# Performance work log

Hardware: AMD Instinct MI355X
Metric: run time of the kernel (lower is better)

## Reference

```python
import jax, jax.numpy as jnp
import numpy as np

B_SZ, L, H, P, V, OUT_LEN = 32, 4096, 512, 384, 32, 16
DT_MIN, DT_MAX = 0.001, 0.1


def setup_inputs() -> dict:
    key = jax.random.key(0)
    ks = jax.random.split(key, 12)
    tokens = jax.random.randint(ks[0], (B_SZ, L), 0, V, dtype=jnp.int32)
    embed = jax.random.normal(ks[1], (V, H), dtype=jnp.float32) * 0.02
    # S5 diagonal state: Lambda = Lambda_re + i*Lambda_im (stable: Re < 0)
    Lambda_re = -0.5 * jax.random.uniform(ks[2], (P,), dtype=jnp.float32) - 1e-3
    Lambda_im = jnp.pi * jnp.arange(P, dtype=jnp.float32)
    B_re = jax.random.normal(ks[3], (P, H), dtype=jnp.float32) / np.sqrt(H)
    B_im = jax.random.normal(ks[4], (P, H), dtype=jnp.float32) / np.sqrt(H)
    C_re = jax.random.normal(ks[5], (H, P), dtype=jnp.float32) / np.sqrt(P)
    C_im = jax.random.normal(ks[6], (H, P), dtype=jnp.float32) / np.sqrt(P)
    D = jax.random.normal(ks[7], (H,), dtype=jnp.float32)
    log_step = jax.random.uniform(
        ks[8], (P,), dtype=jnp.float32,
        minval=np.log(DT_MIN), maxval=np.log(DT_MAX))
    W1 = jax.random.normal(ks[9], (H, H), dtype=jnp.float32) / np.sqrt(H)
    b1 = jnp.zeros((H,), dtype=jnp.float32)
    W2 = jax.random.normal(ks[10], (H, V), dtype=jnp.float32) / np.sqrt(H)
    b2 = jnp.zeros((V,), dtype=jnp.float32)
    return dict(tokens=tokens, embed=embed, Lambda_re=Lambda_re,
                Lambda_im=Lambda_im, B_re=B_re, B_im=B_im, C_re=C_re,
                C_im=C_im, D=D, log_step=log_step, W1=W1, b1=b1, W2=W2, b2=b2)


def _s5_scan(Lbar, Bu_bar):
    # Lbar: (P,) complex; Bu_bar: (B,L,P) complex
    A = jnp.broadcast_to(Lbar, Bu_bar.shape)

    def comb(e1, e2):
        A1, b1 = e1
        A2, b2 = e2
        return A2 * A1, A2 * b1 + b2

    _, xs = jax.lax.associative_scan(comb, (A, Bu_bar), axis=1)
    return xs  # (B,L,P) hidden states


def reference(tokens, embed, Lambda_re, Lambda_im, B_re, B_im,
              C_re, C_im, D, log_step, W1, b1, W2, b2):
    u = embed[tokens]                              # (B,L,H) real
    Lam = Lambda_re + 1j * Lambda_im               # (P,)
    step = jnp.exp(log_step)                       # (P,)
    Lbar = jnp.exp(Lam * step)                     # ZOH: exp(Lambda*dt)
    Bc = B_re + 1j * B_im                          # (P,H)
    Cc = C_re + 1j * C_im                          # (H,P)
    Bu = jnp.einsum('blh,ph->blp', u, Bc)          # (B,L,P) complex
    Bu_bar = ((Lbar - 1.0) / Lam) * Bu             # ZOH input discretization
    xs = _s5_scan(Lbar, Bu_bar)                    # (B,L,P)
    # conj_sym=True -> 2 * Re(C x) + D u
    y = 2.0 * jnp.einsum('blp,hp->blh', xs, Cc).real + u * D
    y = y[:, -OUT_LEN:, :]                         # (B,16,H)
    h = jax.nn.relu(y @ W1 + b1)
    return h @ W2 + b2                             # (B,16,V)
```

## Files before the change

kernel.cpp:

```cpp
#include <hip/hip_runtime.h>

#define B_SZ 32
#define L 4096
#define H 512
#define P 384
#define V 32
#define OUT_LEN 16
#define NSC 12
#define SCLEN 340
#define NSTEP 85
#define T0 4080

#define OFF_DBL   0
#define OFF_LBF4  4608
#define OFF_WPOW  5376
#define OFF_M     23808
#define OFF_CT    48384
#define OFF_XACC  441600
#define OFF_YT    466176
#define OFF_HP    728320

__global__ __launch_bounds__(256) void k_prep(
    const float* __restrict__ embed,
    const float* __restrict__ Lre, const float* __restrict__ Lim,
    const float* __restrict__ Bre, const float* __restrict__ Bim,
    const float* __restrict__ Cre, const float* __restrict__ Cim,
    const float* __restrict__ log_step, float* __restrict__ ws)
{
    __shared__ float sre[32][33], sim[32][33];
    int bx = blockIdx.x, tid = threadIdx.x;
    if (bx < 96) ws[OFF_XACC + bx * 256 + tid] = 0.f;
    if (bx < 2) {
        int p = bx * 256 + tid;
        if (p < P) {
            double dstep = exp((double)log_step[p]);
            double are = (double)Lre[p] * dstep, aim = (double)Lim[p] * dstep;
            double mag = exp(are);
            double lbr = mag * cos(aim), lbi = mag * sin(aim);
            double lre = (double)Lre[p], lim = (double)Lim[p];
            double nr = lbr - 1.0, ni = lbi;
            double den = lre * lre + lim * lim;
            double cr = (nr * lre + ni * lim) / den, ci = (ni * lre - nr * lim) / den;
            double* d = (double*)ws + p * 6;
            d[0] = lbr; d[1] = lbi; d[2] = 0.0; d[3] = 0.0; d[4] = cr; d[5] = ci;
            double m4 = exp(4.0 * are), a4 = 4.0 * aim;
            ws[OFF_LBF4 + 2 * p]     = (float)(m4 * cos(a4));
            ws[OFF_LBF4 + 2 * p + 1] = (float)(m4 * sin(a4));
            double wmag = exp((double)SCLEN * are);
            double wang = (double)SCLEN * aim;
            double wr = wmag * cos(wang), wi = wmag * sin(wang);
            double* wpow = (double*)(ws + OFF_WPOW);
            double awr = 1.0, awi = 0.0;
            for (int c = NSC - 1; c >= 0; --c) {
                wpow[(c * P + p) * 2]     = awr;
                wpow[(c * P + p) * 2 + 1] = awi;
                double t = awr * wr - awi * wi;
                awi = awr * wi + awi * wr;
                awr = t;
            }
        }
    } else if (bx < 194) {
        int bxx = bx - 2;
        int tp = bxx >> 4, th = bxx & 15;
        int col = tid & 31, r0 = tid >> 5;
        #pragma unroll
        for (int it = 0; it < 4; ++it) {
            int row = r0 + 8 * it;
            int h = th * 32 + row, p = tp * 32 + col;
            sre[col][row] = Cre[h * P + p];
            sim[col][row] = Cim[h * P + p];
        }
        __syncthreads();
        #pragma unroll
        for (int it = 0; it < 4; ++it) {
            int pl = r0 + 8 * it;
            int p = tp * 32 + pl, h = th * 32 + col;
            ws[OFF_CT + (2 * p) * H + h]     = sre[pl][col];
            ws[OFF_CT + (2 * p + 1) * H + h] = sim[pl][col];
        }
    }
    {
        int w = bx * 4 + (tid >> 6);
        if (w < 1536) {
            int v0 = (w & 3) * 8, p = w >> 2;
            int lane = tid & 63;
            const float4* brp = (const float4*)(Bre + p * H);
            const float4* bip = (const float4*)(Bim + p * H);
            float4 br0 = brp[lane], br1 = brp[lane + 64];
            float4 bi0 = bip[lane], bi1 = bip[lane + 64];
            #pragma unroll
            for (int vv = 0; vv < 8; ++vv) {
                const float4* evp = (const float4*)(embed + (v0 + vv) * H);
                float4 e0 = evp[lane], e1 = evp[lane + 64];
                float dr = br0.x * e0.x;
                dr = fmaf(br0.y, e0.y, dr); dr = fmaf(br0.z, e0.z, dr);
                dr = fmaf(br0.w, e0.w, dr); dr = fmaf(br1.x, e1.x, dr);
                dr = fmaf(br1.y, e1.y, dr); dr = fmaf(br1.z, e1.z, dr);
                dr = fmaf(br1.w, e1.w, dr);
                float di = bi0.x * e0.x;
                di = fmaf(bi0.y, e0.y, di); di = fmaf(bi0.z, e0.z, di);
                di = fmaf(bi0.w, e0.w, di); di = fmaf(bi1.x, e1.x, di);
                di = fmaf(bi1.y, e1.y, di); di = fmaf(bi1.z, e1.z, di);
                di = fmaf(bi1.w, e1.w, di);
                #pragma unroll
                for (int off = 32; off; off >>= 1) {
                    dr += __shfl_down(dr, off);
                    di += __shfl_down(di, off);
                }
                if (lane == 0) {
                    ws[OFF_M + ((v0 + vv) * P + p) * 2]     = dr;
                    ws[OFF_M + ((v0 + vv) * P + p) * 2 + 1] = di;
                }
            }
        }
    }
}

__global__ __launch_bounds__(256) void k_scan(
    const int* __restrict__ tokens, float* __restrict__ ws)
{
    __shared__ float2 sM[V * 192];
    int x = blockIdx.x, b = blockIdx.y, tid = threadIdx.x;
    int ph = x & 1;
    int sc = x >> 1;
    const float2* Mg = (const float2*)(ws + OFF_M);
    for (int f = tid; f < V * 192; f += 256) {
        int v = f / 192, i = f - v * 192;
        sM[f] = Mg[v * P + ph * 192 + i];
    }
    __syncthreads();
    if (tid < 192) {
        int p = ph * 192 + tid;
        float Lr = ws[OFF_LBF4 + 2 * p], Li = ws[OFF_LBF4 + 2 * p + 1];
        const int4* tkb = (const int4*)(tokens + b * L + sc * SCLEN);
        float ar0 = 0, ai0 = 0, ar1 = 0, ai1 = 0;
        float ar2 = 0, ai2 = 0, ar3 = 0, ai3 = 0;
        int4 tq = tkb[0];
        #pragma unroll 5
        for (int i = 0; i < NSTEP; ++i) {
            int4 cur = tq;
            if (i + 1 < NSTEP) tq = tkb[i + 1];
            float2 m0 = sM[cur.x * 192 + tid];
            float2 m1 = sM[cur.y * 192 + tid];
            float2 m2 = sM[cur.z * 192 + tid];
            float2 m3 = sM[cur.w * 192 + tid];
            float n;
            n = fmaf(Lr, ar0, fmaf(-Li, ai0, m0.x));
            ai0 = fmaf(Lr, ai0, fmaf(Li, ar0, m0.y)); ar0 = n;
            n = fmaf(Lr, ar1, fmaf(-Li, ai1, m1.x));
            ai1 = fmaf(Lr, ai1, fmaf(Li, ar1, m1.y)); ar1 = n;
            n = fmaf(Lr, ar2, fmaf(-Li, ai2, m2.x));
            ai2 = fmaf(Lr, ai2, fmaf(Li, ar2, m2.y)); ar2 = n;
            n = fmaf(Lr, ar3, fmaf(-Li, ai3, m3.x));
            ai3 = fmaf(Lr, ai3, fmaf(Li, ar3, m3.y)); ar3 = n;
        }
        const double* d = (const double*)ws + p * 6;
        double l1r = d[0], l1i = d[1];
        double l2r = l1r * l1r - l1i * l1i, l2i = 2.0 * l1r * l1i;
        double l3r = l2r * l1r - l2i * l1i, l3i = l2r * l1i + l2i * l1r;
        double zr = l3r * ar0 - l3i * ai0 + l2r * ar1 - l2i * ai1
                  + l1r * ar2 - l1i * ai2 + (double)ar3;
        double zi = l3r * ai0 + l3i * ar0 + l2r * ai1 + l2i * ar1
                  + l1r * ai2 + l1i * ar2 + (double)ai3;
        const double* wpow = (const double*)(ws + OFF_WPOW);
        double wr = wpow[(sc * P + p) * 2], wi = wpow[(sc * P + p) * 2 + 1];
        float sr = (float)(wr * zr - wi * zi);
        float si = (float)(wr * zi + wi * zr);
        atomicAdd(ws + OFF_XACC + (b * P + p) * 2, sr);
        atomicAdd(ws + OFF_XACC + (b * P + p) * 2 + 1, si);
    }
}

__global__ __launch_bounds__(256) void k_y(
    const int* __restrict__ tokens, const float* __restrict__ embed,
    const float* __restrict__ D, float* __restrict__ ws)
{
    __shared__ __align__(16) float sxs[P * 20];
    __shared__ float sred[4 * 64 * 9];
    int bx = blockIdx.x, tid = threadIdx.x;
    int b = bx >> 4, x = bx & 15;
    int lh = x & 1, hq = x >> 1;
    #pragma unroll
    for (int pass = 0; pass < 2; ++pass) {
        int p = tid + pass * 256;
        if (p < P) {
            const double* d = (const double*)ws + p * 6;
            double lbr = d[0], lbi = d[1], cr = d[4], ci = d[5];
            const float2 za = *(const float2*)(ws + OFF_XACC + (b * P + p) * 2);
            double zr = (double)za.x, zi = (double)za.y;
            const float* M0 = ws + OFF_M;
            const int* tk = tokens + b * L + T0;
            #pragma unroll
            for (int j = 0; j < OUT_LEN; ++j) {
                int t = tk[j];
                double mr = (double)M0[(t * P + p) * 2];
                double mi = (double)M0[(t * P + p) * 2 + 1];
                double tr = lbr * zr - lbi * zi + mr;
                double ti = lbr * zi + lbi * zr + mi;
                zr = tr; zi = ti;
                if ((j >> 3) == lh) {
                    int jl = j & 7;
                    sxs[p * 20 + 2 * jl]     = (float)(cr * zr - ci * zi);
                    sxs[p * 20 + 2 * jl + 1] = (float)(cr * zi + ci * zr);
                }
            }
        }
    }
    __syncthreads();
    int hl = tid & 63, pg = tid >> 6;
    int h = hq * 64 + hl;
    const float* ct = ws + OFF_CT;
    float acc[8];
    #pragma unroll
    for (int i = 0; i < 8; ++i) acc[i] = 0.f;
    int p0 = pg * 96;
    float pr_[4], pi_[4];
    #pragma unroll
    for (int u = 0; u < 4; ++u) {
        pr_[u] = ct[(2 * (p0 + u)) * H + h];
        pi_[u] = ct[(2 * (p0 + u) + 1) * H + h];
    }
    for (int qs = 0; qs < 96; qs += 4) {
        float cr_[4], ci_[4];
        #pragma unroll
        for (int u = 0; u < 4; ++u) { cr_[u] = pr_[u]; ci_[u] = pi_[u]; }
        if (qs + 4 < 96) {
            #pragma unroll
            for (int u = 0; u < 4; ++u) {
                pr_[u] = ct[(2 * (p0 + qs + 4 + u)) * H + h];
                pi_[u] = ct[(2 * (p0 + qs + 4 + u) + 1) * H + h];
            }
        }
        #pragma unroll
        for (int u = 0; u < 4; ++u) {
            const float4* xv = (const float4*)(sxs + (p0 + qs + u) * 20);
            float4 x0 = xv[0], x1 = xv[1], x2 = xv[2], x3 = xv[3];
            float cre = cr_[u], cim = ci_[u];
            acc[0] = fmaf(cre, x0.x, fmaf(-cim, x0.y, acc[0]));
            acc[1] = fmaf(cre, x0.z, fmaf(-cim, x0.w, acc[1]));
            acc[2] = fmaf(cre, x1.x, fmaf(-cim, x1.y, acc[2]));
            acc[3] = fmaf(cre, x1.z, fmaf(-cim, x1.w, acc[3]));
            acc[4] = fmaf(cre, x2.x, fmaf(-cim, x2.y, acc[4]));
            acc[5] = fmaf(cre, x2.z, fmaf(-cim, x2.w, acc[5]));
            acc[6] = fmaf(cre, x3.x, fmaf(-cim, x3.y, acc[6]));
            acc[7] = fmaf(cre, x3.z, fmaf(-cim, x3.w, acc[7]));
        }
    }
    #pragma unroll
    for (int i = 0; i < 8; ++i)
        sred[(pg * 64 + hl) * 9 + i] = acc[i];
    __syncthreads();
    #pragma unroll
    for (int oo = 0; oo < 2; ++oo) {
        int o = tid + 256 * oo;
        int ohl = o & 63, oi = o >> 6;
        float s = sred[ohl * 9 + oi] + sred[(64 + ohl) * 9 + oi]
                + sred[(128 + ohl) * 9 + oi] + sred[(192 + ohl) * 9 + oi];
        int l = lh * 8 + oi;
        int t = tokens[b * L + T0 + l];
        int hh = hq * 64 + ohl;
        ws[OFF_YT + (b * OUT_LEN + l) * H + hh] =
            2.f * s + embed[t * H + hh] * D[hh];
    }
}

__global__ __launch_bounds__(256) void k_fc1(
    const float* __restrict__ W1, const float* __restrict__ ws,
    float* __restrict__ hp)
{
    __shared__ __align__(16) float ys[64 * 16];
    int bx = blockIdx.x, tid = threadIdx.x;
    int rg = bx >> 4, jh = (bx >> 3) & 1, kc = bx & 7;
    int j = jh * 256 + tid;
    int r0 = rg * 16, k0 = kc * 64;
    const float* yt = ws + OFF_YT;
    int row = tid & 15, kk4 = tid >> 4;
    #pragma unroll
    for (int it = 0; it < 4; ++it) {
        int k = kk4 + 16 * it;
        ys[k * 16 + row] = yt[(r0 + row) * H + k0 + k];
    }
    __syncthreads();
    const float* wp = W1 + k0 * H + j;
    float wreg[8];
    #pragma unroll
    for (int u = 0; u < 8; ++u) wreg[u] = wp[u * H];
    float acc[16];
    #pragma unroll
    for (int i = 0; i < 16; ++i) acc[i] = 0.f;
    for (int kb = 0; kb < 64; kb += 8) {
        float cur[8];
        #pragma unroll
        for (int u = 0; u < 8; ++u) cur[u] = wreg[u];
        if (kb + 8 < 64) {
            #pragma unroll
            for (int u = 0; u < 8; ++u) wreg[u] = wp[(kb + 8 + u) * H];
        }
        #pragma unroll
        for (int u = 0; u < 8; ++u) {
            const float4* y0 = (const float4*)(ys + (kb + u) * 16);
            float4 p0 = y0[0], p1 = y0[1], p2 = y0[2], p3 = y0[3];
            float a = cur[u];
            acc[0]  = fmaf(p0.x, a, acc[0]);
            acc[1]  = fmaf(p0.y, a, acc[1]);
            acc[2]  = fmaf(p0.z, a, acc[2]);
            acc[3]  = fmaf(p0.w, a, acc[3]);
            acc[4]  = fmaf(p1.x, a, acc[4]);
            acc[5]  = fmaf(p1.y, a, acc[5]);
            acc[6]  = fmaf(p1.z, a, acc[6]);
            acc[7]  = fmaf(p1.w, a, acc[7]);
            acc[8]  = fmaf(p2.x, a, acc[8]);
            acc[9]  = fmaf(p2.y, a, acc[9]);
            acc[10] = fmaf(p2.z, a, acc[10]);
            acc[11] = fmaf(p2.w, a, acc[11]);
            acc[12] = fmaf(p3.x, a, acc[12]);
            acc[13] = fmaf(p3.y, a, acc[13]);
            acc[14] = fmaf(p3.z, a, acc[14]);
            acc[15] = fmaf(p3.w, a, acc[15]);
        }
    }
    #pragma unroll
    for (int i = 0; i < 16; ++i)
        hp[(kc * 512 + r0 + i) * H + j] = acc[i];
}

__global__ __launch_bounds__(256) void k_fc2(
    const float* __restrict__ b1, const float* __restrict__ W2,
    const float* __restrict__ b2, const float* __restrict__ hp,
    float* __restrict__ out)
{
    __shared__ float sh[512];
    __shared__ float red[8 * 32];
    int r = blockIdx.x, tid = threadIdx.x;
    #pragma unroll
    for (int half = 0; half < 2; ++half) {
        int j = half * 256 + tid;
        float s = b1[j];
        #pragma unroll
        for (int m = 0; m < 8; ++m)
            s += hp[(m * 512 + r) * H + j];
        sh[j] = fmaxf(s, 0.f);
    }
    __syncthreads();
    int seg = tid >> 5, o = tid & 31;
    const float* w2 = W2 + seg * 64 * V + o;
    const float* hv = sh + seg * 64;
    float a0 = 0.f, a1 = 0.f, a2 = 0.f, a3 = 0.f;
    #pragma unroll
    for (int q = 0; q < 16; ++q) {
        a0 = fmaf(hv[q],      w2[q * V],        a0);
        a1 = fmaf(hv[16 + q], w2[(16 + q) * V], a1);
        a2 = fmaf(hv[32 + q], w2[(32 + q) * V], a2);
        a3 = fmaf(hv[48 + q], w2[(48 + q) * V], a3);
    }
    red[seg * 32 + o] = (a0 + a1) + (a2 + a3);
    __syncthreads();
    if (tid < 32) {
        float s = b2[tid];
        #pragma unroll
        for (int ss = 0; ss < 8; ++ss) s += red[ss * 32 + tid];
        out[r * V + tid] = s;
    }
}

extern "C" void kernel_launch(void* const* d_in, const int* in_sizes, int n_in,
                              void* d_out, int out_size, void* d_ws, size_t ws_size,
                              hipStream_t stream)
{
    const int*   tokens = (const int*)d_in[0];
    const float* embed  = (const float*)d_in[1];
    const float* Lre    = (const float*)d_in[2];
    const float* Lim    = (const float*)d_in[3];
    const float* Bre    = (const float*)d_in[4];
    const float* Bim    = (const float*)d_in[5];
    const float* Cre    = (const float*)d_in[6];
    const float* Cim    = (const float*)d_in[7];
    const float* D      = (const float*)d_in[8];
    const float* lstep  = (const float*)d_in[9];
    const float* W1     = (const float*)d_in[10];
    const float* b1     = (const float*)d_in[11];
    const float* W2     = (const float*)d_in[12];
    const float* b2     = (const float*)d_in[13];
    float* out = (float*)d_out;
    float* ws  = (float*)d_ws;

    k_prep<<<384, 256, 0, stream>>>(embed, Lre, Lim, Bre, Bim,
                                    Cre, Cim, lstep, ws);
    k_scan<<<dim3(24, 32), 256, 0, stream>>>(tokens, ws);
    k_y   <<<512, 256, 0, stream>>>(tokens, embed, D, ws);
    k_fc1 <<<512, 256, 0, stream>>>(W1, ws, ws + OFF_HP);
    k_fc2 <<<512, 256, 0, stream>>>(b1, W2, b2, ws + OFF_HP, out);
}
```

Before: 142.6 us.

## Split tail recurrence into separate kernel to avoid redundant per-block recomputation

The final 16-step double-precision recurrence producing C-projected hidden states was recomputed inside every k_y block, 16 times per batch row across its h-quarter and l-half blocks. A new k_tail kernel computes it once per (batch, state) pair and writes the results to a new global workspace region. k_y now reads those values from global memory instead of building them in shared memory. This trades the redundant FP64 work for an extra kernel launch, a global write and read round trip, and a shift of the YT/HP workspace offsets.

```diff
diff --git a/kernel.cpp b/kernel.cpp
--- a/kernel.cpp
+++ b/kernel.cpp
@@ -17,8 +17,9 @@
 #define OFF_M     23808
 #define OFF_CT    48384
 #define OFF_XACC  441600
-#define OFF_YT    466176
-#define OFF_HP    728320
+#define OFF_XS    466176
+#define OFF_YT    859392
+#define OFF_HP    1121536
 
 __global__ __launch_bounds__(256) void k_prep(
     const float* __restrict__ embed,
@@ -171,45 +172,43 @@
     }
 }
 
+__global__ __launch_bounds__(64) void k_tail(
+    const int* __restrict__ tokens, float* __restrict__ ws)
+{
+    int id = blockIdx.x * 64 + threadIdx.x;
+    int b = id / P, p = id - b * P;
+    const double* d = (const double*)ws + p * 6;
+    double lbr = d[0], lbi = d[1], cr = d[4], ci = d[5];
+    const float2 za = *(const float2*)(ws + OFF_XACC + (b * P + p) * 2);
+    double zr = (double)za.x, zi = (double)za.y;
+    const float* M0 = ws + OFF_M;
+    const int* tk = tokens + b * L + T0;
+    float* xs = ws + OFF_XS + (b * P + p) * 32;
+    #pragma unroll
+    for (int j = 0; j < OUT_LEN; ++j) {
+        int t = tk[j];
+        double mr = (double)M0[(t * P + p) * 2];
+        double mi = (double)M0[(t * P + p) * 2 + 1];
+        double tr = lbr * zr - lbi * zi + mr;
+        double ti = lbr * zi + lbi * zr + mi;
+        zr = tr; zi = ti;
+        xs[2 * j]     = (float)(cr * zr - ci * zi);
+        xs[2 * j + 1] = (float)(cr * zi + ci * zr);
+    }
+}
+
 __global__ __launch_bounds__(256) void k_y(
     const int* __restrict__ tokens, const float* __restrict__ embed,
-    const float* __restrict__ D, float* __restrict__ ws)
-{
-    __shared__ __align__(16) float sxs[P * 20];
+    const float* __restrict__ D, const float* __restrict__ xs,
+    const float* __restrict__ ct, float* __restrict__ yt)
+{
     __shared__ float sred[4 * 64 * 9];
     int bx = blockIdx.x, tid = threadIdx.x;
     int b = bx >> 4, x = bx & 15;
     int lh = x & 1, hq = x >> 1;
-    #pragma unroll
-    for (int pass = 0; pass < 2; ++pass) {
-        int p = tid + pass * 256;
-        if (p < P) {
-            const double* d = (const double*)ws + p * 6;
-            double lbr = d[0], lbi = d[1], cr = d[4], ci = d[5];
-            const float2 za = *(const float2*)(ws + OFF_XACC + (b * P + p) * 2);
-            double zr = (double)za.x, zi = (double)za.y;
-            const float* M0 = ws + OFF_M;
-            const int* tk = tokens + b * L + T0;
-            #pragma unroll
-            for (int j = 0; j < OUT_LEN; ++j) {
-                int t = tk[j];
-                double mr = (double)M0[(t * P + p) * 2];
-                double mi = (double)M0[(t * P + p) * 2 + 1];
-                double tr = lbr * zr - lbi * zi + mr;
-                double ti = lbr * zi + lbi * zr + mi;
-                zr = tr; zi = ti;
-                if ((j >> 3) == lh) {
-                    int jl = j & 7;
-                    sxs[p * 20 + 2 * jl]     = (float)(cr * zr - ci * zi);
-                    sxs[p * 20 + 2 * jl + 1] = (float)(cr * zi + ci * zr);
-                }
-            }
-        }
-    }
-    __syncthreads();
     int hl = tid & 63, pg = tid >> 6;
     int h = hq * 64 + hl;
-    const float* ct = ws + OFF_CT;
+    const float* xb = xs + b * (P * 32) + lh * 16;
     float acc[8];
     #pragma unroll
     for (int i = 0; i < 8; ++i) acc[i] = 0.f;
@@ -233,7 +232,7 @@
         }
         #pragma unroll
         for (int u = 0; u < 4; ++u) {
-            const float4* xv = (const float4*)(sxs + (p0 + qs + u) * 20);
+            const float4* xv = (const float4*)(xb + (p0 + qs + u) * 32);
             float4 x0 = xv[0], x1 = xv[1], x2 = xv[2], x3 = xv[3];
             float cre = cr_[u], cim = ci_[u];
             acc[0] = fmaf(cre, x0.x, fmaf(-cim, x0.y, acc[0]));
@@ -259,7 +258,7 @@
         int l = lh * 8 + oi;
         int t = tokens[b * L + T0 + l];
         int hh = hq * 64 + ohl;
-        ws[OFF_YT + (b * OUT_LEN + l) * H + hh] =
+        yt[(b * OUT_LEN + l) * H + hh] =
             2.f * s + embed[t * H + hh] * D[hh];
     }
 }
@@ -387,7 +386,9 @@
     k_prep<<<384, 256, 0, stream>>>(embed, Lre, Lim, Bre, Bim,
                                     Cre, Cim, lstep, ws);
     k_scan<<<dim3(24, 32), 256, 0, stream>>>(tokens, ws);
-    k_y   <<<512, 256, 0, stream>>>(tokens, embed, D, ws);
+    k_tail<<<192, 64, 0, stream>>>(tokens, ws);
+    k_y   <<<512, 256, 0, stream>>>(tokens, embed, D,
+                                    ws + OFF_XS, ws + OFF_CT, ws + OFF_YT);
     k_fc1 <<<512, 256, 0, stream>>>(W1, ws, ws + OFF_HP);
     k_fc2 <<<512, 256, 0, stream>>>(b1, W2, b2, ws + OFF_HP, out);
 }
```

New measurement: 158.5 us. 11.1% more time.
